# Performance work log

Measured on AMD Instinct MI355X. Metric: run time of the kernel, lower is better.

## Reference

```python
import jax, jax.numpy as jnp
import numpy as np

B, T, N, IN, H, P = 1, 48, 4096, 2, 64, 12


def _normalize_adj(adj):
    A = adj + jnp.eye(adj.shape[0], dtype=adj.dtype)
    d = jnp.sum(A, axis=1)
    dinv = jnp.where(d > 0, d ** -0.5, 0.0)
    return (dinv[:, None] * A) * dinv[None, :]


def _cell(inp, h, c, A, gcWi, gcbi, gcWh, gcbh, liWi, libi, liWh, libh):
    # graph conv: spmm(A, inp @ W) + bias, plus plain linears; all produce [BN, 4H]
    comb = (A @ (inp @ gcWi) + gcbi
            + A @ (h @ gcWh) + gcbh
            + inp @ liWi + libi
            + h @ liWh + libh)
    i_g, f_g, o_g, g_g = jnp.split(comb, 4, axis=1)
    new_c = jax.nn.sigmoid(f_g) * c + jax.nn.sigmoid(i_g) * jnp.tanh(g_g)
    new_h = jax.nn.sigmoid(o_g) * jnp.tanh(new_c)
    return new_h, new_c


def setup_inputs() -> dict:
    key = jax.random.key(0)
    ks = jax.random.split(key, 24)
    s_in = 1.0 / np.sqrt(4 * H)

    def p(k, shape):
        return jax.random.normal(k, shape, dtype=jnp.float32) * s_in

    adj = (jax.random.uniform(ks[1], (N, N)) < 0.01).astype(jnp.float32)
    return {
        "x": jax.random.normal(ks[0], (B, T, N * IN), dtype=jnp.float32),
        "adj": adj,
        "gcWi0": p(ks[2], (IN, 4 * H)), "gcbi0": p(ks[3], (4 * H,)),
        "gcWh0": p(ks[4], (H, 4 * H)), "gcbh0": p(ks[5], (4 * H,)),
        "liWi0": p(ks[6], (IN, 4 * H)), "libi0": p(ks[7], (4 * H,)),
        "liWh0": p(ks[8], (H, 4 * H)), "libh0": p(ks[9], (4 * H,)),
        "gcWi1": p(ks[10], (H, 4 * H)), "gcbi1": p(ks[11], (4 * H,)),
        "gcWh1": p(ks[12], (H, 4 * H)), "gcbh1": p(ks[13], (4 * H,)),
        "liWi1": p(ks[14], (H, 4 * H)), "libi1": p(ks[15], (4 * H,)),
        "liWh1": p(ks[16], (H, 4 * H)), "libh1": p(ks[17], (4 * H,)),
        "outW": p(ks[18], (H, P)), "outb": p(ks[19], (P,)),
    }


def reference(x, adj, gcWi0, gcbi0, gcWh0, gcbh0, liWi0, libi0, liWh0, libh0,
              gcWi1, gcbi1, gcWh1, gcbh1, liWi1, libi1, liWh1, libh1, outW, outb):
    A = _normalize_adj(adj)
    # [B,T,N*IN] -> time-major [T, B*N, IN]
    xs = x.reshape(B, T, N, IN).transpose(1, 0, 2, 3).reshape(T, B * N, IN)
    z = jnp.zeros((B * N, H), dtype=x.dtype)

    def step(carry, xt):
        h0, c0, h1, c1 = carry
        h0, c0 = _cell(xt, h0, c0, A, gcWi0, gcbi0, gcWh0, gcbh0,
                       liWi0, libi0, liWh0, libh0)
        # dropout is identity in eval mode
        h1, c1 = _cell(h0, h1, c1, A, gcWi1, gcbi1, gcWh1, gcbh1,
                       liWi1, libi1, liWh1, libh1)
        return (h0, c0, h1, c1), None

    (h0, c0, h1, c1), _ = jax.lax.scan(step, (z, z, z, z), xs)
    out = h1 @ outW + outb  # [B*N, P]
    return out.reshape(B, N, P)
```

## Files before the change

kernel.cpp:

```cpp
#include <hip/hip_runtime.h>
#include <math.h>

#define NN 4096
#define TT 48
#define HH 64
#define GG 256
#define PP 12
#define CAP 192
#define NH (NN * HH)

__device__ __forceinline__ float bcast_f(float v, int lane) {
  return __int_as_float(__builtin_amdgcn_readlane(__float_as_int(v), lane));
}
__device__ __forceinline__ int bcast_i(int v, int lane) {
  return __builtin_amdgcn_readlane(v, lane);
}

__launch_bounds__(256)
__global__ void k_prep(const float* gcbi0, const float* gcbh0,
                       const float* libi0, const float* libh0,
                       const float* gcbi1, const float* gcbh1,
                       const float* libi1, const float* libh1,
                       const float* gcWh0, const float* liWh0,
                       const float* gcWi1, const float* liWi1,
                       const float* gcWh1, const float* liWh1,
                       const float* gcWi0, const float* liWi0,
                       float* state, float4* Wg0, float4* Wg1,
                       float4* biasg0, float4* biasg1, float4* xq0) {
  int idx = blockIdx.x * 256 + threadIdx.x;
  int stride = gridDim.x * 256;
  for (int i = idx; i < 6 * NH; i += stride) state[i] = 0.0f;
  for (int i = idx; i < 64 * 2 * 64; i += stride) {
    int j = i & 63, m = (i >> 6) & 1, k = i >> 7;
    const float* W = m ? liWh0 : gcWh0;
    Wg0[i] = make_float4(W[k * GG + j], W[k * GG + j + 64],
                         W[k * GG + j + 128], W[k * GG + j + 192]);
  }
  for (int i = idx; i < 64 * 4 * 64; i += stride) {
    int j = i & 63, m = (i >> 6) & 3, k = i >> 8;
    const float* W = (m == 0) ? gcWi1 : (m == 1) ? liWi1 : (m == 2) ? gcWh1 : liWh1;
    Wg1[i] = make_float4(W[k * GG + j], W[k * GG + j + 64],
                         W[k * GG + j + 128], W[k * GG + j + 192]);
  }
  if (idx < 64) {
    int j = idx;
    biasg0[j] = make_float4(
        gcbi0[j] + gcbh0[j] + libi0[j] + libh0[j],
        gcbi0[j + 64] + gcbh0[j + 64] + libi0[j + 64] + libh0[j + 64],
        gcbi0[j + 128] + gcbh0[j + 128] + libi0[j + 128] + libh0[j + 128],
        gcbi0[j + 192] + gcbh0[j + 192] + libi0[j + 192] + libh0[j + 192]);
    biasg1[j] = make_float4(
        gcbi1[j] + gcbh1[j] + libi1[j] + libh1[j],
        gcbi1[j + 64] + gcbh1[j + 64] + libi1[j + 64] + libh1[j + 64],
        gcbi1[j + 128] + gcbh1[j + 128] + libi1[j + 128] + libh1[j + 128],
        gcbi1[j + 192] + gcbh1[j + 192] + libi1[j + 192] + libh1[j + 192]);
  } else if (idx < 320) {
    int i = idx - 64;
    int j = i & 63, m = i >> 6;
    const float* W = (m < 2) ? gcWi0 : liWi0;
    int kk = m & 1;
    xq0[i] = make_float4(W[kk * GG + j], W[kk * GG + j + 64],
                         W[kk * GG + j + 128], W[kk * GG + j + 192]);
  }
}

__launch_bounds__(256)
__global__ void k_build(const float* adj, float* dinv,
                        int* ell_col, float* ell_val, int* ell_cnt) {
  int r = blockIdx.x;
  __shared__ int cnt;
  __shared__ float red[256];
  if (threadIdx.x == 0) cnt = 0;
  __syncthreads();
  const float* row = adj + (size_t)r * NN;
  float s = 0.0f;
  for (int c = threadIdx.x; c < NN; c += 256) {
    float a = row[c];
    if (c == r) a += 1.0f;
    s += a;
    if (a != 0.0f) {
      int pos = atomicAdd(&cnt, 1);
      if (pos < CAP) {
        ell_col[(size_t)r * CAP + pos] = c;
        ell_val[(size_t)r * CAP + pos] = a;
      }
    }
  }
  red[threadIdx.x] = s;
  __syncthreads();
  for (int st = 128; st > 0; st >>= 1) {
    if (threadIdx.x < st) red[threadIdx.x] += red[threadIdx.x + st];
    __syncthreads();
  }
  int n = cnt < CAP ? cnt : CAP;
  for (int j = n + (int)threadIdx.x; j < CAP; j += 256) {
    ell_col[(size_t)r * CAP + j] = 0;
    ell_val[(size_t)r * CAP + j] = 0.0f;
  }
  if (threadIdx.x == 0) {
    int npad = (n + 7) & ~7;
    if (npad > CAP) npad = CAP;
    ell_cnt[r] = npad;
    dinv[r] = 1.0f / sqrtf(red[0]);
  }
}

__launch_bounds__(256)
__global__ void k_scale(const float* dinv, const int* ell_col, float* ell_val) {
  int idx = blockIdx.x * 256 + threadIdx.x;
  int r = idx / CAP;
  if (r >= NN) return;
  float v = ell_val[idx];
  if (v != 0.0f) ell_val[idx] = v * dinv[r] * dinv[ell_col[idx]];
}

__launch_bounds__(256)
__global__ void k_gax(const float* x, const int* ell_col, const float* ell_val,
                      const int* ell_cnt, float* gax) {
  int t = blockIdx.x >> 3;
  int seg = blockIdx.x & 7;
  __shared__ float xs[NN * 2];
  const float* xt = x + (size_t)t * NN * 2;
  for (int i = threadIdx.x; i < NN * 2; i += 256) xs[i] = xt[i];
  __syncthreads();
  int base = seg * 512 * 2;
  for (int oo = threadIdx.x; oo < 512 * 2; oo += 256) {
    int o = base + oo;
    int r = o >> 1, cmp = o & 1;
    int cnt = ell_cnt[r];
    const int* cp = ell_col + (size_t)r * CAP;
    const float* vp = ell_val + (size_t)r * CAP;
    float acc = 0.0f;
    for (int j = 0; j < cnt; j += 4) {
      acc += vp[j]     * xs[cp[j]     * 2 + cmp];
      acc += vp[j + 1] * xs[cp[j + 1] * 2 + cmp];
      acc += vp[j + 2] * xs[cp[j + 2] * 2 + cmp];
      acc += vp[j + 3] * xs[cp[j + 3] * 2 + cmp];
    }
    gax[(size_t)t * NN * 2 + o] = acc;
  }
}

__device__ __forceinline__ void cell0_body(
    int blk, int tid,
    const int* __restrict__ ell_col, const float* __restrict__ ell_val,
    const int* __restrict__ ell_cnt,
    const float2* __restrict__ Pr, float* __restrict__ Pw,
    float* __restrict__ c0,
    const float* __restrict__ xt, const float* __restrict__ gaxt,
    const float4* __restrict__ Wg0, const float4* __restrict__ biasg0,
    const float4* __restrict__ xq0, float4* wbuf) {
  const int wave = tid >> 6, lane = tid & 63;
  const int r0 = blk * 8 + wave * 2;

  const float4* pf = Wg0 + tid;
  float4 st0 = pf[0], st1 = pf[256], st2 = pf[512], st3 = pf[768];
  pf += 1024;

  int myc[2][3]; float myv[2][3]; int cnts[2];
#pragma unroll
  for (int rr = 0; rr < 2; rr++) {
    int r = r0 + rr;
    cnts[rr] = ell_cnt[r];
#pragma unroll
    for (int chk = 0; chk < 3; chk++) {
      myc[rr][chk] = ell_col[(size_t)r * CAP + chk * 64 + lane];
      myv[rr][chk] = ell_val[(size_t)r * CAP + chk * 64 + lane];
    }
  }
  float gacc[2], hl[2];
#pragma unroll
  for (int rr = 0; rr < 2; rr++) {
    int cnt = cnts[rr];
    float acc = 0.0f;
#pragma unroll
    for (int chk = 0; chk < 3; chk++) {
      int base = chk * 64;
      if (base < cnt) {
        int lim = cnt - base; if (lim > 64) lim = 64;
        int mc = myc[rr][chk]; float mv = myv[rr][chk];
        for (int m = 0; m < lim; m += 8) {
          float2 ld[8]; float vv[8];
#pragma unroll
          for (int i = 0; i < 8; i++) {
            int cc = bcast_i(mc, m + i);
            vv[i] = bcast_f(mv, m + i);
            ld[i] = Pr[(size_t)cc * 64 + lane];
          }
#pragma unroll
          for (int i = 0; i < 8; i++) acc += vv[i] * ld[i].x;
        }
      }
    }
    gacc[rr] = acc;
    hl[rr] = Pr[(size_t)(r0 + rr) * 64 + lane].x;
  }

  float4 acc[2];
  {
    float4 b = biasg0[lane];
    float4 qg0 = xq0[lane], qg1 = xq0[64 + lane];
    float4 ql0 = xq0[128 + lane], ql1 = xq0[192 + lane];
#pragma unroll
    for (int rr = 0; rr < 2; rr++) {
      float xx0 = xt[(size_t)(r0 + rr) * 2];
      float xx1 = xt[(size_t)(r0 + rr) * 2 + 1];
      float gg0 = gaxt[(size_t)(r0 + rr) * 2];
      float gg1 = gaxt[(size_t)(r0 + rr) * 2 + 1];
      acc[rr].x = b.x + gg0 * qg0.x + gg1 * qg1.x + xx0 * ql0.x + xx1 * ql1.x;
      acc[rr].y = b.y + gg0 * qg0.y + gg1 * qg1.y + xx0 * ql0.y + xx1 * ql1.y;
      acc[rr].z = b.z + gg0 * qg0.z + gg1 * qg1.z + xx0 * ql0.z + xx1 * ql1.z;
      acc[rr].w = b.w + gg0 * qg0.w + gg1 * qg1.w + xx0 * ql0.w + xx1 * ql1.w;
    }
  }

  wbuf[tid] = st0; wbuf[256 + tid] = st1;
  wbuf[512 + tid] = st2; wbuf[768 + tid] = st3;
  __syncthreads();
  int cur = 0;
#pragma unroll 1
  for (int ch = 0; ch < 8; ch++) {
    if (ch + 1 < 8) {
      st0 = pf[0]; st1 = pf[256]; st2 = pf[512]; st3 = pf[768];
      pf += 1024;
    }
    const float4* wb = wbuf + (cur << 10);
#pragma unroll
    for (int kk = 0; kk < 8; kk++) {
      int k = ch * 8 + kk;
      float4 w0 = wb[(kk * 2 + 0) * 64 + lane];
      float4 w1 = wb[(kk * 2 + 1) * 64 + lane];
#pragma unroll
      for (int rr = 0; rr < 2; rr++) {
        float a0 = bcast_f(gacc[rr], k);
        float a1 = bcast_f(hl[rr], k);
        acc[rr].x += a0 * w0.x + a1 * w1.x;
        acc[rr].y += a0 * w0.y + a1 * w1.y;
        acc[rr].z += a0 * w0.z + a1 * w1.z;
        acc[rr].w += a0 * w0.w + a1 * w1.w;
      }
    }
    if (ch + 1 < 8) {
      cur ^= 1;
      float4* dst = wbuf + (cur << 10) + tid;
      dst[0] = st0; dst[256] = st1; dst[512] = st2; dst[768] = st3;
      __syncthreads();
    }
  }

#pragma unroll
  for (int rr = 0; rr < 2; rr++) {
    size_t gi = (size_t)(r0 + rr) * HH + lane;
    float cprev = c0[gi];
    float si = 1.0f / (1.0f + __expf(-acc[rr].x));
    float sf = 1.0f / (1.0f + __expf(-acc[rr].y));
    float so = 1.0f / (1.0f + __expf(-acc[rr].z));
    float cn = sf * cprev + si * tanhf(acc[rr].w);
    float hn = so * tanhf(cn);
    c0[gi] = cn;
    Pw[gi * 2 + 0] = hn;
  }
}

__device__ __forceinline__ void cell1_body(
    int blk, int tid,
    const int* __restrict__ ell_col, const float* __restrict__ ell_val,
    const int* __restrict__ ell_cnt,
    const float2* __restrict__ Pr, float* __restrict__ Pw,
    float* __restrict__ c1,
    const float4* __restrict__ Wg1, const float4* __restrict__ biasg1,
    float4* wbuf) {
  const int wave = tid >> 6, lane = tid & 63;
  const int r0 = blk * 8 + wave * 2;

  const float4* pf = Wg1 + tid;
  float4 st0 = pf[0], st1 = pf[256], st2 = pf[512], st3 = pf[768];
  pf += 1024;

  int myc[2][3]; float myv[2][3]; int cnts[2];
#pragma unroll
  for (int rr = 0; rr < 2; rr++) {
    int r = r0 + rr;
    cnts[rr] = ell_cnt[r];
#pragma unroll
    for (int chk = 0; chk < 3; chk++) {
      myc[rr][chk] = ell_col[(size_t)r * CAP + chk * 64 + lane];
      myv[rr][chk] = ell_val[(size_t)r * CAP + chk * 64 + lane];
    }
  }
  float ga0[2], ga1[2], hl0[2], hl1[2];
#pragma unroll
  for (int rr = 0; rr < 2; rr++) {
    int cnt = cnts[rr];
    float a0 = 0.0f, a1 = 0.0f;
#pragma unroll
    for (int chk = 0; chk < 3; chk++) {
      int base = chk * 64;
      if (base < cnt) {
        int lim = cnt - base; if (lim > 64) lim = 64;
        int mc = myc[rr][chk]; float mv = myv[rr][chk];
        for (int m = 0; m < lim; m += 8) {
          float2 ld[8]; float vv[8];
#pragma unroll
          for (int i = 0; i < 8; i++) {
            int cc = bcast_i(mc, m + i);
            vv[i] = bcast_f(mv, m + i);
            ld[i] = Pr[(size_t)cc * 64 + lane];
          }
#pragma unroll
          for (int i = 0; i < 8; i++) {
            a0 += vv[i] * ld[i].x;
            a1 += vv[i] * ld[i].y;
          }
        }
      }
    }
    ga0[rr] = a0;
    ga1[rr] = a1;
    float2 hh = Pr[(size_t)(r0 + rr) * 64 + lane];
    hl0[rr] = hh.x;
    hl1[rr] = hh.y;
  }

  float4 acc[2];
  {
    float4 b = biasg1[lane];
    acc[0] = b; acc[1] = b;
  }

  wbuf[tid] = st0; wbuf[256 + tid] = st1;
  wbuf[512 + tid] = st2; wbuf[768 + tid] = st3;
  __syncthreads();
  int cur = 0;
#pragma unroll 1
  for (int ch = 0; ch < 16; ch++) {
    if (ch + 1 < 16) {
      st0 = pf[0]; st1 = pf[256]; st2 = pf[512]; st3 = pf[768];
      pf += 1024;
    }
    const float4* wb = wbuf + (cur << 10);
#pragma unroll
    for (int kk = 0; kk < 4; kk++) {
      int k = ch * 4 + kk;
      float4 w0 = wb[(kk * 4 + 0) * 64 + lane];
      float4 w1 = wb[(kk * 4 + 1) * 64 + lane];
      float4 w2 = wb[(kk * 4 + 2) * 64 + lane];
      float4 w3 = wb[(kk * 4 + 3) * 64 + lane];
#pragma unroll
      for (int rr = 0; rr < 2; rr++) {
        float a0 = bcast_f(ga0[rr], k);
        float a1 = bcast_f(hl0[rr], k);
        float a2 = bcast_f(ga1[rr], k);
        float a3 = bcast_f(hl1[rr], k);
        acc[rr].x += a0 * w0.x + a1 * w1.x + a2 * w2.x + a3 * w3.x;
        acc[rr].y += a0 * w0.y + a1 * w1.y + a2 * w2.y + a3 * w3.y;
        acc[rr].z += a0 * w0.z + a1 * w1.z + a2 * w2.z + a3 * w3.z;
        acc[rr].w += a0 * w0.w + a1 * w1.w + a2 * w2.w + a3 * w3.w;
      }
    }
    if (ch + 1 < 16) {
      cur ^= 1;
      float4* dst = wbuf + (cur << 10) + tid;
      dst[0] = st0; dst[256] = st1; dst[512] = st2; dst[768] = st3;
      __syncthreads();
    }
  }

#pragma unroll
  for (int rr = 0; rr < 2; rr++) {
    size_t gi = (size_t)(r0 + rr) * HH + lane;
    float cprev = c1[gi];
    float si = 1.0f / (1.0f + __expf(-acc[rr].x));
    float sf = 1.0f / (1.0f + __expf(-acc[rr].y));
    float so = 1.0f / (1.0f + __expf(-acc[rr].z));
    float cn = sf * cprev + si * tanhf(acc[rr].w);
    float hn = so * tanhf(cn);
    c1[gi] = cn;
    Pw[gi * 2 + 1] = hn;
  }
}

__launch_bounds__(256)
__global__ void k_cells(int c0blocks,
                        const int* __restrict__ ell_col,
                        const float* __restrict__ ell_val,
                        const int* __restrict__ ell_cnt,
                        const float2* __restrict__ Pr, float* __restrict__ Pw,
                        float* __restrict__ c0, float* __restrict__ c1,
                        const float* __restrict__ xt, const float* __restrict__ gaxt,
                        const float4* __restrict__ Wg0,
                        const float4* __restrict__ biasg0,
                        const float4* __restrict__ xq0,
                        const float4* __restrict__ Wg1,
                        const float4* __restrict__ biasg1) {
  __shared__ float4 wbuf[2048];
  int b = blockIdx.x;
  if (b < c0blocks) {
    cell0_body(b, threadIdx.x, ell_col, ell_val, ell_cnt, Pr, Pw, c0, xt, gaxt,
               Wg0, biasg0, xq0, wbuf);
  } else {
    cell1_body(b - c0blocks, threadIdx.x, ell_col, ell_val, ell_cnt, Pr, Pw, c1,
               Wg1, biasg1, wbuf);
  }
}

__launch_bounds__(256)
__global__ void k_out(const float* __restrict__ P0, const float* __restrict__ outW,
                      const float* __restrict__ outb, float* __restrict__ out) {
  int idx = blockIdx.x * 256 + threadIdx.x;
  if (idx >= NN * PP) return;
  int r = idx / PP, p = idx - r * PP;
  float acc = outb[p];
  const float* hrow = P0 + (size_t)r * 128;
#pragma unroll 16
  for (int k = 0; k < HH; k++) acc += hrow[k * 2 + 1] * outW[k * PP + p];
  out[idx] = acc;
}

extern "C" void kernel_launch(void* const* d_in, const int* in_sizes, int n_in,
                              void* d_out, int out_size, void* d_ws, size_t ws_size,
                              hipStream_t stream) {
  const float* x     = (const float*)d_in[0];
  const float* adj   = (const float*)d_in[1];
  const float* gcWi0 = (const float*)d_in[2];
  const float* gcbi0 = (const float*)d_in[3];
  const float* gcWh0 = (const float*)d_in[4];
  const float* gcbh0 = (const float*)d_in[5];
  const float* liWi0 = (const float*)d_in[6];
  const float* libi0 = (const float*)d_in[7];
  const float* liWh0 = (const float*)d_in[8];
  const float* libh0 = (const float*)d_in[9];
  const float* gcWi1 = (const float*)d_in[10];
  const float* gcbi1 = (const float*)d_in[11];
  const float* gcWh1 = (const float*)d_in[12];
  const float* gcbh1 = (const float*)d_in[13];
  const float* liWi1 = (const float*)d_in[14];
  const float* libi1 = (const float*)d_in[15];
  const float* liWh1 = (const float*)d_in[16];
  const float* libh1 = (const float*)d_in[17];
  const float* outW  = (const float*)d_in[18];
  const float* outb  = (const float*)d_in[19];

  char* ws = (char*)d_ws;
  size_t off = 0;
  auto carve = [&](size_t bytes) {
    void* p = ws + off;
    off += (bytes + 255) & ~(size_t)255;
    return p;
  };
  float*  dinv    = (float*)carve((size_t)NN * 4);
  int*    ell_col = (int*)carve((size_t)NN * CAP * 4);
  float*  ell_val = (float*)carve((size_t)NN * CAP * 4);
  int*    ell_cnt = (int*)carve((size_t)NN * 4);
  float*  state   = (float*)carve((size_t)6 * NH * 4);
  float*  gax     = (float*)carve((size_t)TT * NN * 2 * 4);
  float4* Wg0     = (float4*)carve((size_t)64 * 2 * 64 * 16);
  float4* Wg1     = (float4*)carve((size_t)64 * 4 * 64 * 16);
  float4* biasg0  = (float4*)carve((size_t)64 * 16);
  float4* biasg1  = (float4*)carve((size_t)64 * 16);
  float4* xq0     = (float4*)carve((size_t)256 * 16);

  float* P[2] = {state, state + 2 * NH};
  float* c0 = state + 4 * NH;
  float* c1 = state + 5 * NH;

  k_prep<<<512, 256, 0, stream>>>(gcbi0, gcbh0, libi0, libh0,
                                  gcbi1, gcbh1, libi1, libh1,
                                  gcWh0, liWh0, gcWi1, liWi1, gcWh1, liWh1,
                                  gcWi0, liWi0,
                                  state, Wg0, Wg1, biasg0, biasg1, xq0);
  k_build<<<NN, 256, 0, stream>>>(adj, dinv, ell_col, ell_val, ell_cnt);
  k_scale<<<(NN * CAP) / 256, 256, 0, stream>>>(dinv, ell_col, ell_val);
  k_gax<<<TT * 8, 256, 0, stream>>>(x, ell_col, ell_val, ell_cnt, gax);

  for (int k = 0; k <= TT; k++) {
    int A = k & 1;
    int c0blocks = (k < TT) ? NN / 8 : 0;
    int c1blocks = (k > 0) ? NN / 8 : 0;
    int grid = c0blocks + c1blocks;
    int tx = (k < TT) ? k : (TT - 1);
    k_cells<<<grid, 256, 0, stream>>>(
        c0blocks, ell_col, ell_val, ell_cnt,
        (const float2*)P[A ^ 1], P[A], c0, c1,
        x + (size_t)tx * NN * 2, gax + (size_t)tx * NN * 2,
        Wg0, biasg0, xq0, Wg1, biasg1);
  }

  k_out<<<(NN * PP + 255) / 256, 256, 0, stream>>>(P[0], outW, outb, (float*)d_out);
}
```

Baseline: 1.880 ms.

## Merge layer-0 and layer-1 cell blocks to share one SpMM gather

Before, separate blocks ran cell 0 and cell 1, and each did its own sparse gather over the packed state (h0,h1) for the same rows. Now one block handles both cells for its rows. A single gather accumulates both components, and the weight streaming runs as one continuous double-buffered sweep over concatenated Wg0 and Wg1. This halves the gather traffic and the grid size, but each block does more serial work and the larger grid no longer covers latency as well.

```diff
diff --git a/kernel.cpp b/kernel.cpp
--- a/kernel.cpp
+++ b/kernel.cpp
@@ -141,21 +141,34 @@
   }
 }
 
-__device__ __forceinline__ void cell0_body(
-    int blk, int tid,
-    const int* __restrict__ ell_col, const float* __restrict__ ell_val,
-    const int* __restrict__ ell_cnt,
-    const float2* __restrict__ Pr, float* __restrict__ Pw,
-    float* __restrict__ c0,
-    const float* __restrict__ xt, const float* __restrict__ gaxt,
-    const float4* __restrict__ Wg0, const float4* __restrict__ biasg0,
-    const float4* __restrict__ xq0, float4* wbuf) {
+__launch_bounds__(256)
+__global__ void k_cells(int c0on, int c1on,
+                        const int* __restrict__ ell_col,
+                        const float* __restrict__ ell_val,
+                        const int* __restrict__ ell_cnt,
+                        const float2* __restrict__ Pr, float* __restrict__ Pw,
+                        float* __restrict__ c0, float* __restrict__ c1,
+                        const float* __restrict__ xt, const float* __restrict__ gaxt,
+                        const float4* __restrict__ Wg,
+                        const float4* __restrict__ biasg0,
+                        const float4* __restrict__ xq0,
+                        const float4* __restrict__ biasg1) {
+  __shared__ float4 wbuf[2048];
+  const int tid = threadIdx.x;
   const int wave = tid >> 6, lane = tid & 63;
-  const int r0 = blk * 8 + wave * 2;
-
-  const float4* pf = Wg0 + tid;
+  const int r0 = blockIdx.x * 8 + wave * 2;
+
+  const float4* pf = Wg + tid;
   float4 st0 = pf[0], st1 = pf[256], st2 = pf[512], st3 = pf[768];
   pf += 1024;
+
+  float cprev0[2], cprev1[2];
+#pragma unroll
+  for (int rr = 0; rr < 2; rr++) {
+    size_t gi = (size_t)(r0 + rr) * HH + lane;
+    cprev0[rr] = c0[gi];
+    cprev1[rr] = c1[gi];
+  }
 
   int myc[2][3]; float myv[2][3]; int cnts[2];
 #pragma unroll
@@ -168,11 +181,12 @@
       myv[rr][chk] = ell_val[(size_t)r * CAP + chk * 64 + lane];
     }
   }
-  float gacc[2], hl[2];
+
+  float ga0[2], ga1[2], hl0[2], hl1[2];
 #pragma unroll
   for (int rr = 0; rr < 2; rr++) {
     int cnt = cnts[rr];
-    float acc = 0.0f;
+    float a0 = 0.0f, a1 = 0.0f;
 #pragma unroll
     for (int chk = 0; chk < 3; chk++) {
       int base = chk * 64;
@@ -188,15 +202,21 @@
             ld[i] = Pr[(size_t)cc * 64 + lane];
           }
 #pragma unroll
-          for (int i = 0; i < 8; i++) acc += vv[i] * ld[i].x;
+          for (int i = 0; i < 8; i++) {
+            a0 += vv[i] * ld[i].x;
+            a1 += vv[i] * ld[i].y;
+          }
         }
       }
     }
-    gacc[rr] = acc;
-    hl[rr] = Pr[(size_t)(r0 + rr) * 64 + lane].x;
-  }
-
-  float4 acc[2];
+    ga0[rr] = a0;
+    ga1[rr] = a1;
+    float2 hh = Pr[(size_t)(r0 + rr) * 64 + lane];
+    hl0[rr] = hh.x;
+    hl1[rr] = hh.y;
+  }
+
+  float4 acc0[2], acc1[2];
   {
     float4 b = biasg0[lane];
     float4 qg0 = xq0[lane], qg1 = xq0[64 + lane];
@@ -207,23 +227,24 @@
       float xx1 = xt[(size_t)(r0 + rr) * 2 + 1];
       float gg0 = gaxt[(size_t)(r0 + rr) * 2];
       float gg1 = gaxt[(size_t)(r0 + rr) * 2 + 1];
-      acc[rr].x = b.x + gg0 * qg0.x + gg1 * qg1.x + xx0 * ql0.x + xx1 * ql1.x;
-      acc[rr].y = b.y + gg0 * qg0.y + gg1 * qg1.y + xx0 * ql0.y + xx1 * ql1.y;
-      acc[rr].z = b.z + gg0 * qg0.z + gg1 * qg1.z + xx0 * ql0.z + xx1 * ql1.z;
-      acc[rr].w = b.w + gg0 * qg0.w + gg1 * qg1.w + xx0 * ql0.w + xx1 * ql1.w;
-    }
+      acc0[rr].x = b.x + gg0 * qg0.x + gg1 * qg1.x + xx0 * ql0.x + xx1 * ql1.x;
+      acc0[rr].y = b.y + gg0 * qg0.y + gg1 * qg1.y + xx0 * ql0.y + xx1 * ql1.y;
+      acc0[rr].z = b.z + gg0 * qg0.z + gg1 * qg1.z + xx0 * ql0.z + xx1 * ql1.z;
+      acc0[rr].w = b.w + gg0 * qg0.w + gg1 * qg1.w + xx0 * ql0.w + xx1 * ql1.w;
+    }
+    float4 b1 = biasg1[lane];
+    acc1[0] = b1; acc1[1] = b1;
   }
 
   wbuf[tid] = st0; wbuf[256 + tid] = st1;
   wbuf[512 + tid] = st2; wbuf[768 + tid] = st3;
   __syncthreads();
   int cur = 0;
+
 #pragma unroll 1
   for (int ch = 0; ch < 8; ch++) {
-    if (ch + 1 < 8) {
-      st0 = pf[0]; st1 = pf[256]; st2 = pf[512]; st3 = pf[768];
-      pf += 1024;
-    }
+    st0 = pf[0]; st1 = pf[256]; st2 = pf[512]; st3 = pf[768];
+    pf += 1024;
     const float4* wb = wbuf + (cur << 10);
 #pragma unroll
     for (int kk = 0; kk < 8; kk++) {
@@ -232,175 +253,79 @@
       float4 w1 = wb[(kk * 2 + 1) * 64 + lane];
 #pragma unroll
       for (int rr = 0; rr < 2; rr++) {
-        float a0 = bcast_f(gacc[rr], k);
-        float a1 = bcast_f(hl[rr], k);
-        acc[rr].x += a0 * w0.x + a1 * w1.x;
-        acc[rr].y += a0 * w0.y + a1 * w1.y;
-        acc[rr].z += a0 * w0.z + a1 * w1.z;
-        acc[rr].w += a0 * w0.w + a1 * w1.w;
-      }
-    }
-    if (ch + 1 < 8) {
-      cur ^= 1;
-      float4* dst = wbuf + (cur << 10) + tid;
-      dst[0] = st0; dst[256] = st1; dst[512] = st2; dst[768] = st3;
-      __syncthreads();
-    }
-  }
-
-#pragma unroll
-  for (int rr = 0; rr < 2; rr++) {
-    size_t gi = (size_t)(r0 + rr) * HH + lane;
-    float cprev = c0[gi];
-    float si = 1.0f / (1.0f + __expf(-acc[rr].x));
-    float sf = 1.0f / (1.0f + __expf(-acc[rr].y));
-    float so = 1.0f / (1.0f + __expf(-acc[rr].z));
-    float cn = sf * cprev + si * tanhf(acc[rr].w);
-    float hn = so * tanhf(cn);
-    c0[gi] = cn;
-    Pw[gi * 2 + 0] = hn;
-  }
-}
-
-__device__ __forceinline__ void cell1_body(
-    int blk, int tid,
-    const int* __restrict__ ell_col, const float* __restrict__ ell_val,
-    const int* __restrict__ ell_cnt,
-    const float2* __restrict__ Pr, float* __restrict__ Pw,
-    float* __restrict__ c1,
-    const float4* __restrict__ Wg1, const float4* __restrict__ biasg1,
-    float4* wbuf) {
-  const int wave = tid >> 6, lane = tid & 63;
-  const int r0 = blk * 8 + wave * 2;
-
-  const float4* pf = Wg1 + tid;
-  float4 st0 = pf[0], st1 = pf[256], st2 = pf[512], st3 = pf[768];
-  pf += 1024;
-
-  int myc[2][3]; float myv[2][3]; int cnts[2];
-#pragma unroll
-  for (int rr = 0; rr < 2; rr++) {
-    int r = r0 + rr;
-    cnts[rr] = ell_cnt[r];
-#pragma unroll
-    for (int chk = 0; chk < 3; chk++) {
-      myc[rr][chk] = ell_col[(size_t)r * CAP + chk * 64 + lane];
-      myv[rr][chk] = ell_val[(size_t)r * CAP + chk * 64 + lane];
-    }
-  }
-  float ga0[2], ga1[2], hl0[2], hl1[2];
-#pragma unroll
-  for (int rr = 0; rr < 2; rr++) {
-    int cnt = cnts[rr];
-    float a0 = 0.0f, a1 = 0.0f;
-#pragma unroll
-    for (int chk = 0; chk < 3; chk++) {
-      int base = chk * 64;
-      if (base < cnt) {
-        int lim = cnt - base; if (lim > 64) lim = 64;
-        int mc = myc[rr][chk]; float mv = myv[rr][chk];
-        for (int m = 0; m < lim; m += 8) {
-          float2 ld[8]; float vv[8];
-#pragma unroll
-          for (int i = 0; i < 8; i++) {
-            int cc = bcast_i(mc, m + i);
-            vv[i] = bcast_f(mv, m + i);
-            ld[i] = Pr[(size_t)cc * 64 + lane];
-          }
-#pragma unroll
-          for (int i = 0; i < 8; i++) {
-            a0 += vv[i] * ld[i].x;
-            a1 += vv[i] * ld[i].y;
-          }
-        }
-      }
-    }
-    ga0[rr] = a0;
-    ga1[rr] = a1;
-    float2 hh = Pr[(size_t)(r0 + rr) * 64 + lane];
-    hl0[rr] = hh.x;
-    hl1[rr] = hh.y;
-  }
-
-  float4 acc[2];
-  {
-    float4 b = biasg1[lane];
-    acc[0] = b; acc[1] = b;
-  }
-
-  wbuf[tid] = st0; wbuf[256 + tid] = st1;
-  wbuf[512 + tid] = st2; wbuf[768 + tid] = st3;
-  __syncthreads();
-  int cur = 0;
-#pragma unroll 1
-  for (int ch = 0; ch < 16; ch++) {
-    if (ch + 1 < 16) {
-      st0 = pf[0]; st1 = pf[256]; st2 = pf[512]; st3 = pf[768];
-      pf += 1024;
-    }
-    const float4* wb = wbuf + (cur << 10);
-#pragma unroll
-    for (int kk = 0; kk < 4; kk++) {
-      int k = ch * 4 + kk;
-      float4 w0 = wb[(kk * 4 + 0) * 64 + lane];
-      float4 w1 = wb[(kk * 4 + 1) * 64 + lane];
-      float4 w2 = wb[(kk * 4 + 2) * 64 + lane];
-      float4 w3 = wb[(kk * 4 + 3) * 64 + lane];
-#pragma unroll
-      for (int rr = 0; rr < 2; rr++) {
         float a0 = bcast_f(ga0[rr], k);
         float a1 = bcast_f(hl0[rr], k);
-        float a2 = bcast_f(ga1[rr], k);
-        float a3 = bcast_f(hl1[rr], k);
-        acc[rr].x += a0 * w0.x + a1 * w1.x + a2 * w2.x + a3 * w3.x;
-        acc[rr].y += a0 * w0.y + a1 * w1.y + a2 * w2.y + a3 * w3.y;
-        acc[rr].z += a0 * w0.z + a1 * w1.z + a2 * w2.z + a3 * w3.z;
-        acc[rr].w += a0 * w0.w + a1 * w1.w + a2 * w2.w + a3 * w3.w;
-      }
-    }
-    if (ch + 1 < 16) {
-      cur ^= 1;
-      float4* dst = wbuf + (cur << 10) + tid;
-      dst[0] = st0; dst[256] = st1; dst[512] = st2; dst[768] = st3;
-      __syncthreads();
-    }
-  }
-
-#pragma unroll
-  for (int rr = 0; rr < 2; rr++) {
-    size_t gi = (size_t)(r0 + rr) * HH + lane;
-    float cprev = c1[gi];
-    float si = 1.0f / (1.0f + __expf(-acc[rr].x));
-    float sf = 1.0f / (1.0f + __expf(-acc[rr].y));
-    float so = 1.0f / (1.0f + __expf(-acc[rr].z));
-    float cn = sf * cprev + si * tanhf(acc[rr].w);
-    float hn = so * tanhf(cn);
-    c1[gi] = cn;
-    Pw[gi * 2 + 1] = hn;
-  }
-}
-
-__launch_bounds__(256)
-__global__ void k_cells(int c0blocks,
-                        const int* __restrict__ ell_col,
-                        const float* __restrict__ ell_val,
-                        const int* __restrict__ ell_cnt,
-                        const float2* __restrict__ Pr, float* __restrict__ Pw,
-                        float* __restrict__ c0, float* __restrict__ c1,
-                        const float* __restrict__ xt, const float* __restrict__ gaxt,
-                        const float4* __restrict__ Wg0,
-                        const float4* __restrict__ biasg0,
-                        const float4* __restrict__ xq0,
-                        const float4* __restrict__ Wg1,
-                        const float4* __restrict__ biasg1) {
-  __shared__ float4 wbuf[2048];
-  int b = blockIdx.x;
-  if (b < c0blocks) {
-    cell0_body(b, threadIdx.x, ell_col, ell_val, ell_cnt, Pr, Pw, c0, xt, gaxt,
-               Wg0, biasg0, xq0, wbuf);
-  } else {
-    cell1_body(b - c0blocks, threadIdx.x, ell_col, ell_val, ell_cnt, Pr, Pw, c1,
-               Wg1, biasg1, wbuf);
+        acc0[rr].x += a0 * w0.x + a1 * w1.x;
+        acc0[rr].y += a0 * w0.y + a1 * w1.y;
+        acc0[rr].z += a0 * w0.z + a1 * w1.z;
+        acc0[rr].w += a0 * w0.w + a1 * w1.w;
+      }
+    }
+    cur ^= 1;
+    float4* dst = wbuf + (cur << 10) + tid;
+    dst[0] = st0; dst[256] = st1; dst[512] = st2; dst[768] = st3;
+    __syncthreads();
+  }
+
+  if (c0on) {
+#pragma unroll
+    for (int rr = 0; rr < 2; rr++) {
+      size_t gi = (size_t)(r0 + rr) * HH + lane;
+      float si = 1.0f / (1.0f + __expf(-acc0[rr].x));
+      float sf = 1.0f / (1.0f + __expf(-acc0[rr].y));
+      float so = 1.0f / (1.0f + __expf(-acc0[rr].z));
+      float cn = sf * cprev0[rr] + si * tanhf(acc0[rr].w);
+      float hn = so * tanhf(cn);
+      c0[gi] = cn;
+      Pw[gi * 2 + 0] = hn;
+    }
+  }
+
+  if (c1on) {
+#pragma unroll 1
+    for (int ch = 0; ch < 16; ch++) {
+      if (ch + 1 < 16) {
+        st0 = pf[0]; st1 = pf[256]; st2 = pf[512]; st3 = pf[768];
+        pf += 1024;
+      }
+      const float4* wb = wbuf + (cur << 10);
+#pragma unroll
+      for (int kk = 0; kk < 4; kk++) {
+        int k = ch * 4 + kk;
+        float4 w0 = wb[(kk * 4 + 0) * 64 + lane];
+        float4 w1 = wb[(kk * 4 + 1) * 64 + lane];
+        float4 w2 = wb[(kk * 4 + 2) * 64 + lane];
+        float4 w3 = wb[(kk * 4 + 3) * 64 + lane];
+#pragma unroll
+        for (int rr = 0; rr < 2; rr++) {
+          float a0 = bcast_f(ga0[rr], k);
+          float a1 = bcast_f(hl0[rr], k);
+          float a2 = bcast_f(ga1[rr], k);
+          float a3 = bcast_f(hl1[rr], k);
+          acc1[rr].x += a0 * w0.x + a1 * w1.x + a2 * w2.x + a3 * w3.x;
+          acc1[rr].y += a0 * w0.y + a1 * w1.y + a2 * w2.y + a3 * w3.y;
+          acc1[rr].z += a0 * w0.z + a1 * w1.z + a2 * w2.z + a3 * w3.z;
+          acc1[rr].w += a0 * w0.w + a1 * w1.w + a2 * w2.w + a3 * w3.w;
+        }
+      }
+      if (ch + 1 < 16) {
+        cur ^= 1;
+        float4* dst = wbuf + (cur << 10) + tid;
+        dst[0] = st0; dst[256] = st1; dst[512] = st2; dst[768] = st3;
+        __syncthreads();
+      }
+    }
+#pragma unroll
+    for (int rr = 0; rr < 2; rr++) {
+      size_t gi = (size_t)(r0 + rr) * HH + lane;
+      float si = 1.0f / (1.0f + __expf(-acc1[rr].x));
+      float sf = 1.0f / (1.0f + __expf(-acc1[rr].y));
+      float so = 1.0f / (1.0f + __expf(-acc1[rr].z));
+      float cn = sf * cprev1[rr] + si * tanhf(acc1[rr].w);
+      float hn = so * tanhf(cn);
+      c1[gi] = cn;
+      Pw[gi * 2 + 1] = hn;
+    }
   }
 }
 
@@ -454,12 +379,13 @@
   int*    ell_cnt = (int*)carve((size_t)NN * 4);
   float*  state   = (float*)carve((size_t)6 * NH * 4);
   float*  gax     = (float*)carve((size_t)TT * NN * 2 * 4);
-  float4* Wg0     = (float4*)carve((size_t)64 * 2 * 64 * 16);
-  float4* Wg1     = (float4*)carve((size_t)64 * 4 * 64 * 16);
+  float4* Wgm     = (float4*)carve((size_t)(8192 + 16384) * 16);
   float4* biasg0  = (float4*)carve((size_t)64 * 16);
   float4* biasg1  = (float4*)carve((size_t)64 * 16);
   float4* xq0     = (float4*)carve((size_t)256 * 16);
 
+  float4* Wg0 = Wgm;
+  float4* Wg1 = Wgm + 8192;
   float* P[2] = {state, state + 2 * NH};
   float* c0 = state + 4 * NH;
   float* c1 = state + 5 * NH;
@@ -475,15 +401,14 @@
 
   for (int k = 0; k <= TT; k++) {
     int A = k & 1;
-    int c0blocks = (k < TT) ? NN / 8 : 0;
-    int c1blocks = (k > 0) ? NN / 8 : 0;
-    int grid = c0blocks + c1blocks;
+    int c0on = (k < TT) ? 1 : 0;
+    int c1on = (k > 0) ? 1 : 0;
     int tx = (k < TT) ? k : (TT - 1);
-    k_cells<<<grid, 256, 0, stream>>>(
-        c0blocks, ell_col, ell_val, ell_cnt,
+    k_cells<<<NN / 8, 256, 0, stream>>>(
+        c0on, c1on, ell_col, ell_val, ell_cnt,
         (const float2*)P[A ^ 1], P[A], c0, c1,
         x + (size_t)tx * NN * 2, gax + (size_t)tx * NN * 2,
-        Wg0, biasg0, xq0, Wg1, biasg1);
+        Wgm, biasg0, xq0, biasg1);
   }
 
   k_out<<<(NN * PP + 255) / 256, 256, 0, stream>>>(P[0], outW, outb, (float*)d_out);
```

Result: faster. 1.797 ms (-4.4%).
